# Kernel tuning notes

Hardware: AMD Instinct MI355X
Metric: run time of the kernel (lower is better)

## Reference

```python
import jax, jax.numpy as jnp
import numpy as np

NUM_LAYERS = 5
EMB = 300
N_GRAPHS = 4096
BN_EPS = 1e-5
TEMP = 0.04


def _gnn_encode(x, edge_index, edge_attr, atom_emb1, atom_emb2,
                edge_emb1, edge_emb2, mlp_w1, mlp_b1, mlp_w2, mlp_b2,
                bn_gamma, bn_beta):
    n = x.shape[0]
    h = atom_emb1[x[:, 0]] + atom_emb2[x[:, 1]]  # [N, EMB]
    src, dst = edge_index[0], edge_index[1]
    for l in range(NUM_LAYERS):
        eemb = edge_emb1[l][edge_attr[:, 0]] + edge_emb2[l][edge_attr[:, 1]]  # [E, EMB]
        self_emb = edge_emb1[l][4] + edge_emb2[l][0]  # self-loop edge_attr = [4, 0]
        agg = jax.ops.segment_sum(h[src] + eemb, dst, num_segments=n)
        agg = agg + h + self_emb  # self-loop messages
        h = jax.nn.relu(agg @ mlp_w1[l] + mlp_b1[l]) @ mlp_w2[l] + mlp_b2[l]
        mean = jnp.mean(h, axis=0)
        var = jnp.var(h, axis=0)
        h = (h - mean) / jnp.sqrt(var + BN_EPS) * bn_gamma[l] + bn_beta[l]
        if l != NUM_LAYERS - 1:
            h = jax.nn.relu(h)
    return h


def _branch(x, edge_index, edge_attr, node_batch, params):
    h = _gnn_encode(x, edge_index, edge_attr, *params[:-2])
    h = h @ params[-2] + params[-1]  # projector
    s = jax.ops.segment_sum(h, node_batch, num_segments=N_GRAPHS)
    cnt = jax.ops.segment_sum(jnp.ones((h.shape[0],), h.dtype), node_batch,
                              num_segments=N_GRAPHS)
    g = s / jnp.maximum(cnt, 1.0)[:, None]  # global mean pool
    norm = jnp.maximum(jnp.linalg.norm(g, axis=1, keepdims=True), 1e-12)
    return g / norm


def setup_inputs() -> dict:
    key = jax.random.key(0)
    ks = jax.random.split(key, 24)
    f = jnp.float32
    inp = {}
    inp['x0'] = jax.random.randint(ks[0], (100000, 2), 0, 3)
    inp['edge_index0'] = jax.random.randint(ks[1], (2, 400000), 0, 100000)
    inp['edge_attr0'] = jax.random.randint(ks[2], (400000, 2), 0, 3)
    inp['batch0'] = jnp.sort(jax.random.randint(ks[3], (100000,), 0, N_GRAPHS))
    inp['x1'] = jax.random.randint(ks[4], (100000, 2), 0, 3)
    inp['edge_index1'] = jax.random.randint(ks[5], (2, 400000), 0, 100000)
    inp['edge_attr1'] = jax.random.randint(ks[6], (400000, 2), 0, 3)
    inp['batch1'] = jnp.sort(jax.random.randint(ks[7], (100000,), 0, N_GRAPHS))
    s = 0.02
    inp['atom_emb1'] = jax.random.normal(ks[8], (120, EMB), f) * s
    inp['atom_emb2'] = jax.random.normal(ks[9], (3, EMB), f) * s
    inp['edge_emb1'] = jax.random.normal(ks[10], (NUM_LAYERS, 6, EMB), f) * s
    inp['edge_emb2'] = jax.random.normal(ks[11], (NUM_LAYERS, 3, EMB), f) * s
    inp['mlp_w1'] = jax.random.normal(ks[12], (NUM_LAYERS, EMB, 2 * EMB), f) * s
    inp['mlp_b1'] = jnp.zeros((NUM_LAYERS, 2 * EMB), f)
    inp['mlp_w2'] = jax.random.normal(ks[13], (NUM_LAYERS, 2 * EMB, EMB), f) * s
    inp['mlp_b2'] = jnp.zeros((NUM_LAYERS, EMB), f)
    inp['bn_gamma'] = jnp.ones((NUM_LAYERS, EMB), f)
    inp['bn_beta'] = jnp.zeros((NUM_LAYERS, EMB), f)
    inp['proj_w'] = jax.random.normal(ks[14], (EMB, EMB), f) * s
    inp['proj_b'] = jnp.zeros((EMB,), f)
    return inp


def reference(x0, edge_index0, edge_attr0, batch0,
              x1, edge_index1, edge_attr1, batch1,
              atom_emb1, atom_emb2, edge_emb1, edge_emb2,
              mlp_w1, mlp_b1, mlp_w2, mlp_b2, bn_gamma, bn_beta,
              proj_w, proj_b):
    params = (atom_emb1, atom_emb2, edge_emb1, edge_emb2,
              mlp_w1, mlp_b1, mlp_w2, mlp_b2, bn_gamma, bn_beta,
              proj_w, proj_b)
    f0 = _branch(x0, edge_index0, edge_attr0, batch0, params)
    f1 = _branch(x1, edge_index1, edge_attr1, batch1, params)
    logits = (f0 @ f1.T) / TEMP  # [G, G]
    return logits
```

## Files before the change

### kernel.cpp

```cpp
#include <hip/hip_runtime.h>
#include <hip/hip_bf16.h>


#define EMB 300
#define EMBC 75
#define AGGP 320
#define AGGC 80
#define HID 600
#define NGRAPH 4096
#define BN_EPS 1e-5f
#define INV_TEMP 25.0f
#define NRED 24

typedef __hip_bfloat16 bf16;
struct __align__(8) bf4 { bf16 x, y, z, w; };
typedef __attribute__((ext_vector_type(8))) short short8;
typedef __attribute__((ext_vector_type(4))) float float4v;

__device__ inline float b2f(bf16 v) { return __bfloat162float(v); }
__device__ inline bf16 f2b(float v) { return __float2bfloat16(v); }
__device__ inline unsigned short f2bu(float f) {
    bf16 b = __float2bfloat16(f); unsigned short u; __builtin_memcpy(&u, &b, 2); return u;
}

typedef const unsigned int __attribute__((address_space(1)))* gas_t;
typedef unsigned int __attribute__((address_space(3)))* las_t;
__device__ __forceinline__ void gl_lds16(const unsigned short* g, unsigned short* l) {
    __builtin_amdgcn_global_load_lds((gas_t)g, (las_t)l, 16, 0, 0);
}


__global__ void k_zero_f(float* __restrict__ p, int n) {
    int i = blockIdx.x * blockDim.x + threadIdx.x;
    if (i < n) p[i] = 0.f;
}
__global__ void k_zero_i(int* __restrict__ p, int n) {
    int i = blockIdx.x * blockDim.x + threadIdx.x;
    if (i < n) p[i] = 0;
}


__global__ void k_split(const float* __restrict__ W, int K, int N, int Kpad, int Npad,
                        unsigned short* __restrict__ hi, unsigned short* __restrict__ lo) {
    int idx = blockIdx.x * blockDim.x + threadIdx.x;
    if (idx >= Npad * Kpad) return;
    int n = idx / Kpad, k = idx % Kpad;
    float v = (n < N && k < K) ? W[(size_t)k * N + n] : 0.f;
    bf16 h = __float2bfloat16(v);
    float rem = v - __bfloat162float(h);
    bf16 l = __float2bfloat16(rem);
    unsigned short hu, lu;
    __builtin_memcpy(&hu, &h, 2); __builtin_memcpy(&lu, &l, 2);
    hi[idx] = hu; lo[idx] = lu;
}

__global__ void k_fsplit(const float* __restrict__ f, unsigned short* __restrict__ hi,
                         unsigned short* __restrict__ lo, int G) {
    int idx = blockIdx.x * blockDim.x + threadIdx.x;
    if (idx >= G * AGGP) return;
    int g = idx / AGGP, c = idx % AGGP;
    float v = (c < EMB) ? f[(size_t)g * EMB + c] : 0.f;
    bf16 h = __float2bfloat16(v);
    float rem = v - __bfloat162float(h);
    unsigned short hu; __builtin_memcpy(&hu, &h, 2);
    hi[idx] = hu;
    lo[idx] = f2bu(rem);
}


__global__ void k_hist(const int* __restrict__ ei, int* __restrict__ deg, int E) {
    int e = blockIdx.x * blockDim.x + threadIdx.x;
    if (e < E) atomicAdd(&deg[ei[E + e]], 1);
}

__global__ void k_chunksum(const int* __restrict__ deg, int* __restrict__ csum, int total) {
    __shared__ int s[256];
    int t = threadIdx.x, i = blockIdx.x * 256 + t;
    s[t] = (i < total) ? deg[i] : 0;
    __syncthreads();
    for (int off = 128; off > 0; off >>= 1) {
        if (t < off) s[t] += s[t + off];
        __syncthreads();
    }
    if (t == 0) csum[blockIdx.x] = s[0];
}

__global__ void k_scanchunks(const int* __restrict__ csum, int* __restrict__ coff, int n) {
    if (threadIdx.x == 0) {
        int acc = 0;
        for (int b = 0; b < n; ++b) { coff[b] = acc; acc += csum[b]; }
    }
}

__global__ void k_scan2(const int* __restrict__ deg, const int* __restrict__ coff,
                        int* __restrict__ rowstart, int total) {
    __shared__ int s[256];
    int t = threadIdx.x, b = blockIdx.x, i = b * 256 + t;
    int v = (i < total) ? deg[i] : 0;
    s[t] = v;
    __syncthreads();
    for (int off = 1; off < 256; off <<= 1) {
        int u = (t >= off) ? s[t - off] : 0;
        __syncthreads();
        s[t] += u;
        __syncthreads();
    }
    if (i < total) rowstart[i] = coff[b] + s[t] - v;
}

__global__ void k_initcursor(const int* __restrict__ rowstart, int* __restrict__ cur, int N) {
    int i = blockIdx.x * blockDim.x + threadIdx.x;
    if (i < N) cur[i] = rowstart[i];
}

__global__ void k_fill(const int* __restrict__ ei, int* __restrict__ cur,
                       int* __restrict__ esorted, int E) {
    int e = blockIdx.x * blockDim.x + threadIdx.x;
    if (e < E) {
        int p = atomicAdd(&cur[ei[E + e]], 1);
        esorted[p] = e;
    }
}

__global__ void k_pack(const int* __restrict__ ei, const int* __restrict__ ea,
                       const int* __restrict__ esorted, int* __restrict__ packed, int E) {
    int p = blockIdx.x * blockDim.x + threadIdx.x;
    if (p >= E) return;
    int e = esorted[p];
    int s = ei[e];
    int cb = ea[2 * e] * 3 + ea[2 * e + 1];
    packed[p] = s | (cb << 17);
}

__global__ void k_sortb(const int* __restrict__ rowstart, int* __restrict__ packed, int N) {
    int n = blockIdx.x * blockDim.x + threadIdx.x;
    if (n >= N) return;
    int p0 = rowstart[n], p1 = rowstart[n + 1];
    for (int i = p0 + 1; i < p1; ++i) {
        int v = packed[i];
        int j = i - 1;
        while (j >= p0 && packed[j] > v) { packed[j + 1] = packed[j]; --j; }
        packed[j + 1] = v;
    }
}

__global__ void k_gstart(const int* __restrict__ batch, int* __restrict__ gstart, int N) {
    int g = blockIdx.x * blockDim.x + threadIdx.x;
    if (g > NGRAPH) return;
    int lo = 0, hi = N;
    while (lo < hi) { int mid = (lo + hi) >> 1; if (batch[mid] < g) lo = mid + 1; else hi = mid; }
    gstart[g] = lo;
}

__global__ void k_combo(const float4* __restrict__ e1, const float4* __restrict__ e2,
                        float4* __restrict__ cmb) {
    int t = blockIdx.x * blockDim.x + threadIdx.x;
    if (t >= 18 * EMBC) return;
    int cb = t / EMBC, j = t % EMBC;
    float4 u = e1[(cb / 3) * EMBC + j];
    float4 v = e2[(cb % 3) * EMBC + j];
    float4 r; r.x = u.x + v.x; r.y = u.y + v.y; r.z = u.z + v.z; r.w = u.w + v.w;
    cmb[t] = r;
}


__global__ void k_init_h(const int* __restrict__ x,
                         const float4* __restrict__ ae1,
                         const float4* __restrict__ ae2,
                         bf4* __restrict__ h4, int N) {
    int idx = blockIdx.x * blockDim.x + threadIdx.x;
    if (idx >= N * EMBC) return;
    int i = idx / EMBC, j = idx % EMBC;
    int a0 = x[2 * i], a1 = x[2 * i + 1];
    float4 u = ae1[a0 * EMBC + j];
    float4 v = ae2[a1 * EMBC + j];
    bf4 r = { f2b(u.x + v.x), f2b(u.y + v.y), f2b(u.z + v.z), f2b(u.w + v.w) };
    h4[idx] = r;
}

__global__ void k_aggregate(const bf4* __restrict__ h4,
                            const int* __restrict__ packed,
                            const float4* __restrict__ cmb,
                            const int* __restrict__ rowstart,
                            const float* __restrict__ stats, int use_aff,
                            bf4* __restrict__ agg4, int N) {
    int idx = blockIdx.x * blockDim.x + threadIdx.x;
    if (idx >= N * AGGC) return;
    int n = idx / AGGC, j = idx % AGGC;
    if (j >= EMBC) {
        bf4 z = { f2b(0.f), f2b(0.f), f2b(0.f), f2b(0.f) };
        agg4[idx] = z;
        return;
    }
    float4 sc = make_float4(1.f, 1.f, 1.f, 1.f);
    float4 sh = make_float4(0.f, 0.f, 0.f, 0.f);
    if (use_aff) {
        sc = ((const float4*)stats)[j];
        sh = ((const float4*)(stats + EMB))[j];
    }
    bf4 hv = h4[(size_t)n * EMBC + j];
    float hx = b2f(hv.x), hy = b2f(hv.y), hz = b2f(hv.z), hw = b2f(hv.w);
    if (use_aff) {
        hx = fmaxf(hx * sc.x + sh.x, 0.f); hy = fmaxf(hy * sc.y + sh.y, 0.f);
        hz = fmaxf(hz * sc.z + sh.z, 0.f); hw = fmaxf(hw * sc.w + sh.w, 0.f);
    }
    float4 s0 = cmb[12 * EMBC + j];
    float ax = hx + s0.x, ay = hy + s0.y, az = hz + s0.z, aw = hw + s0.w;
    int p0 = rowstart[n], p1 = rowstart[n + 1];
    for (int p = p0; p < p1; ++p) {
        int u = packed[p];
        int s = u & 131071;
        int cb = u >> 17;
        bf4 hs = h4[(size_t)s * EMBC + j];
        float gx = b2f(hs.x), gy = b2f(hs.y), gz = b2f(hs.z), gw = b2f(hs.w);
        if (use_aff) {
            gx = fmaxf(gx * sc.x + sh.x, 0.f); gy = fmaxf(gy * sc.y + sh.y, 0.f);
            gz = fmaxf(gz * sc.z + sh.z, 0.f); gw = fmaxf(gw * sc.w + sh.w, 0.f);
        }
        float4 cv = cmb[cb * EMBC + j];
        ax += gx + cv.x; ay += gy + cv.y;
        az += gz + cv.z; aw += gw + cv.w;
    }
    bf4 r = { f2b(ax), f2b(ay), f2b(az), f2b(aw) };
    agg4[idx] = r;
}

__global__ void k_bncopy(const bf4* __restrict__ h4, const float* __restrict__ stats,
                         bf4* __restrict__ dst, int N) {
    int idx = blockIdx.x * blockDim.x + threadIdx.x;
    if (idx >= N * AGGC) return;
    int n = idx / AGGC, j = idx % AGGC;
    if (j >= EMBC) {
        bf4 z = { f2b(0.f), f2b(0.f), f2b(0.f), f2b(0.f) };
        dst[idx] = z;
        return;
    }
    float4 sc = ((const float4*)stats)[j];
    float4 sh = ((const float4*)(stats + EMB))[j];
    bf4 v = h4[(size_t)n * EMBC + j];
    bf4 r = { f2b(b2f(v.x) * sc.x + sh.x), f2b(b2f(v.y) * sc.y + sh.y),
              f2b(b2f(v.z) * sc.z + sh.z), f2b(b2f(v.w) * sc.w + sh.w) };
    dst[idx] = r;
}


#define GBM 128
#define GBN 64
#define GBK 32

__global__ __launch_bounds__(256, 5)
void k_gemm_mfma(const unsigned short* __restrict__ A, int lda, int Kpad,
                 const unsigned short* __restrict__ Bhi,
                 const unsigned short* __restrict__ Blo, int ldb,
                 const float* __restrict__ bias,
                 unsigned short* __restrict__ C, int ldc, int M, int Nc, int relu,
                 float* __restrict__ psum, int do_stats) {
    __shared__ unsigned short As[2][GBM][GBK];
    __shared__ unsigned short Bh[2][GBN][GBK];
    __shared__ unsigned short Bl[2][GBN][GBK];

    int tid = threadIdx.x;
    int wv = tid >> 6, lane = tid & 63;
    int quad = lane >> 4, l16 = lane & 15;
    int wm = wv & 1, wn = wv >> 1;

    int srow = lane >> 2;
    int gch = (lane & 3) ^ ((lane >> 3) & 3);
    int pc = quad ^ ((l16 >> 1) & 3);

    int ncols = gridDim.x, nrows = gridDim.y;
    int lin = blockIdx.y * ncols + blockIdx.x;
    int g = lin / (8 * ncols);
    int rem = lin - g * 8 * ncols;
    int rows_in = min(8, nrows - g * 8);
    int colb = rem / rows_in;
    int rowb = g * 8 + (rem - colb * rows_in);
    int row0 = rowb * GBM;
    int col0 = colb * GBN;

    const unsigned short* Asrc[2];
    #pragma unroll
    for (int j = 0; j < 2; ++j) {
        int r = 32 * wv + 16 * j + srow;
        Asrc[j] = A + (size_t)min(row0 + r, M - 1) * lda + gch * 8;
    }
    const unsigned short* Bsrc = Bhi + (size_t)(col0 + 16 * wv + srow) * ldb + gch * 8;
    const size_t dBL = (size_t)(Blo - Bhi);

    float4v acc[4][2];
    #pragma unroll
    for (int i = 0; i < 4; ++i)
        #pragma unroll
        for (int j = 0; j < 2; ++j) acc[i][j] = (float4v){0.f, 0.f, 0.f, 0.f};

    const int ntk = Kpad / GBK;

    gl_lds16(Asrc[0], &As[0][32 * wv][0]);
    gl_lds16(Asrc[1], &As[0][32 * wv + 16][0]);
    gl_lds16(Bsrc, &Bh[0][16 * wv][0]);
    gl_lds16(Bsrc + dBL, &Bl[0][16 * wv][0]);
    if (ntk > 1) {
        gl_lds16(Asrc[0] + GBK, &As[1][32 * wv][0]);
        gl_lds16(Asrc[1] + GBK, &As[1][32 * wv + 16][0]);
        gl_lds16(Bsrc + GBK, &Bh[1][16 * wv][0]);
        gl_lds16(Bsrc + GBK + dBL, &Bl[1][16 * wv][0]);
    }

    for (int t = 0; t < ntk; ++t) {
        int cur = t & 1;
        if (t + 1 < ntk) {
            asm volatile("s_waitcnt vmcnt(4)" ::: "memory");
        } else {
            asm volatile("s_waitcnt vmcnt(0)" ::: "memory");
        }
        __builtin_amdgcn_s_barrier();
        __builtin_amdgcn_sched_barrier(0);
        short8 a[4];
        #pragma unroll
        for (int mt = 0; mt < 4; ++mt)
            a[mt] = *(const short8*)(&As[cur][64 * wm + mt * 16 + l16][pc * 8]);
        #pragma unroll
        for (int ntl = 0; ntl < 2; ++ntl) {
            short8 bh = *(const short8*)(&Bh[cur][32 * wn + ntl * 16 + l16][pc * 8]);
            short8 bl = *(const short8*)(&Bl[cur][32 * wn + ntl * 16 + l16][pc * 8]);
            #pragma unroll
            for (int mt = 0; mt < 4; ++mt) {
                acc[mt][ntl] = __builtin_amdgcn_mfma_f32_16x16x32_bf16(a[mt], bh, acc[mt][ntl], 0, 0, 0);
                acc[mt][ntl] = __builtin_amdgcn_mfma_f32_16x16x32_bf16(a[mt], bl, acc[mt][ntl], 0, 0, 0);
            }
        }
        __builtin_amdgcn_s_barrier();
        __builtin_amdgcn_sched_barrier(0);
        if (t + 2 < ntk) {
            int k2 = (t + 2) * GBK;
            gl_lds16(Asrc[0] + k2, &As[cur][32 * wv][0]);
            gl_lds16(Asrc[1] + k2, &As[cur][32 * wv + 16][0]);
            gl_lds16(Bsrc + k2, &Bh[cur][16 * wv][0]);
            gl_lds16(Bsrc + k2 + dBL, &Bl[cur][16 * wv][0]);
        }
    }

    float sv[2], qv[2];
    #pragma unroll
    for (int ntl = 0; ntl < 2; ++ntl) { sv[ntl] = 0.f; qv[ntl] = 0.f; }
    #pragma unroll
    for (int mt = 0; mt < 4; ++mt) {
        int rbase = row0 + 64 * wm + mt * 16 + quad * 4;
        #pragma unroll
        for (int ntl = 0; ntl < 2; ++ntl) {
            int c = col0 + 32 * wn + ntl * 16 + l16;
            if (c >= Nc) continue;
            float bs = bias[c];
            #pragma unroll
            for (int i = 0; i < 4; ++i) {
                int r = rbase + i;
                if (r >= M) continue;
                float v = acc[mt][ntl][i] + bs;
                if (relu) v = fmaxf(v, 0.f);
                if (do_stats) { sv[ntl] += v; qv[ntl] += v * v; }
                C[(size_t)r * ldc + c] = f2bu(v);
            }
        }
    }
    if (do_stats) {
        float* cred = (float*)(&As[0][0][0]);
        #pragma unroll
        for (int ntl = 0; ntl < 2; ++ntl) {
            float s = sv[ntl], q = qv[ntl];
            s += __shfl_down(s, 32, 64); s += __shfl_down(s, 16, 64);
            q += __shfl_down(q, 32, 64); q += __shfl_down(q, 16, 64);
            if (quad == 0) {
                cred[wv * 64 + ntl * 16 + l16] = s;
                cred[256 + wv * 64 + ntl * 16 + l16] = q;
            }
        }
        __syncthreads();
        if (tid < 64) {
            int gc = tid >> 5, cin = tid & 31;
            float s = cred[(2 * gc) * 64 + cin] + cred[(2 * gc + 1) * 64 + cin];
            float q = cred[256 + (2 * gc) * 64 + cin] + cred[256 + (2 * gc + 1) * 64 + cin];
            int c = col0 + tid;
            psum[(size_t)rowb * 768 + c] = s;
            psum[(size_t)rowb * 768 + 384 + c] = q;
        }
    }
}


__global__ __launch_bounds__(256)
void k_logits(const unsigned short* __restrict__ Ahg, const unsigned short* __restrict__ Alg,
              const unsigned short* __restrict__ Bhg, const unsigned short* __restrict__ Blg,
              float* __restrict__ C, float scale) {
    __shared__ unsigned short sAh[64][64];
    __shared__ unsigned short sAl[64][64];
    __shared__ unsigned short sBh[128][64];
    __shared__ unsigned short sBl[128][64];

    int tid = threadIdx.x;
    int wv = tid >> 6, lane = tid & 63;
    int quad = lane >> 4, l16 = lane & 15;
    int lrow = lane >> 3;
    int gchunk = (lane & 7) ^ lrow;
    int sw = lane & 7;
    int row0 = blockIdx.y * 64;
    int col0 = blockIdx.x * 128;

    float4v acc[8];
    #pragma unroll
    for (int j = 0; j < 8; ++j) acc[j] = (float4v){0.f, 0.f, 0.f, 0.f};

    for (int k0 = 0; k0 < AGGP; k0 += 64) {
        #pragma unroll
        for (int j = 0; j < 2; ++j) {
            int r = 16 * wv + 8 * j + lrow;
            size_t go = (size_t)(row0 + r) * AGGP + k0 + gchunk * 8;
            gl_lds16(Ahg + go, &sAh[16 * wv + 8 * j][0]);
            gl_lds16(Alg + go, &sAl[16 * wv + 8 * j][0]);
        }
        #pragma unroll
        for (int j = 0; j < 4; ++j) {
            int r = 32 * wv + 8 * j + lrow;
            size_t go = (size_t)(col0 + r) * AGGP + k0 + gchunk * 8;
            gl_lds16(Bhg + go, &sBh[32 * wv + 8 * j][0]);
            gl_lds16(Blg + go, &sBl[32 * wv + 8 * j][0]);
        }
        __syncthreads();

        #pragma unroll
        for (int ks = 0; ks < 64; ks += 32) {
            int pcl = ((ks >> 3) + quad) ^ sw;
            short8 ah = *(const short8*)(&sAh[wv * 16 + l16][pcl * 8]);
            short8 al = *(const short8*)(&sAl[wv * 16 + l16][pcl * 8]);
            #pragma unroll
            for (int nt = 0; nt < 8; ++nt) {
                short8 bh = *(const short8*)(&sBh[nt * 16 + l16][pcl * 8]);
                short8 bl = *(const short8*)(&sBl[nt * 16 + l16][pcl * 8]);
                acc[nt] = __builtin_amdgcn_mfma_f32_16x16x32_bf16(ah, bh, acc[nt], 0, 0, 0);
                acc[nt] = __builtin_amdgcn_mfma_f32_16x16x32_bf16(ah, bl, acc[nt], 0, 0, 0);
                acc[nt] = __builtin_amdgcn_mfma_f32_16x16x32_bf16(al, bh, acc[nt], 0, 0, 0);
            }
        }
        __syncthreads();
    }

    int rbase = row0 + wv * 16 + quad * 4;
    #pragma unroll
    for (int nt = 0; nt < 8; ++nt) {
        int c = col0 + nt * 16 + l16;
        #pragma unroll
        for (int i = 0; i < 4; ++i)
            C[(size_t)(rbase + i) * NGRAPH + c] = acc[nt][i] * scale;
    }
}


__global__ void k_statred(const float* __restrict__ psum, float* __restrict__ part2, int nrb) {
    int b = blockIdx.x, c = threadIdx.x;
    float acc = 0.f;
    for (int r = b; r < nrb; r += NRED) acc += psum[(size_t)r * 768 + c];
    part2[b * 768 + c] = acc;
}

__global__ void k_bn_prep(const float* __restrict__ part2, float* __restrict__ stats,
                          const float* __restrict__ gamma, const float* __restrict__ beta,
                          float invN) {
    int c = threadIdx.x;
    if (c >= EMB) return;
    float s = 0.f, q = 0.f;
    for (int b = 0; b < NRED; ++b) {
        s += part2[b * 768 + c];
        q += part2[b * 768 + 384 + c];
    }
    float mean = s * invN;
    float var = q * invN - mean * mean;
    float scale = gamma[c] * rsqrtf(var + BN_EPS);
    stats[c] = scale;
    stats[EMB + c] = beta[c] - mean * scale;
}


__global__ void k_poolnorm(const bf16* __restrict__ proj, const int* __restrict__ gstart,
                           float* __restrict__ f) {
    int g = blockIdx.x, t = threadIdx.x;
    int s = gstart[g], e = gstart[g + 1];
    float sum = 0.f;
    if (t < EMB)
        for (int r = s; r < e; ++r) sum += b2f(proj[(size_t)r * AGGP + t]);
    float cnt = fmaxf((float)(e - s), 1.f);
    float m = sum / cnt;
    float q = (t < EMB) ? m * m : 0.f;
    for (int off = 32; off > 0; off >>= 1) q += __shfl_down(q, off, 64);
    __shared__ float red[5];
    int lane = t & 63, wid = t >> 6;
    if (lane == 0) red[wid] = q;
    __syncthreads();
    float tot = red[0] + red[1] + red[2] + red[3] + red[4];
    float invn = 1.f / fmaxf(sqrtf(tot), 1e-12f);
    if (t < EMB) f[(size_t)g * EMB + t] = m * invn;
}


static inline int ceil_div(int a, int b) { return (a + b - 1) / b; }

extern "C" void kernel_launch(void* const* d_in, const int* in_sizes, int n_in,
                              void* d_out, int out_size, void* d_ws, size_t ws_size,
                              hipStream_t stream) {
    const int N = in_sizes[0] / 2;
    const int E = in_sizes[1] / 2;

    const int* x[2]  = { (const int*)d_in[0], (const int*)d_in[4] };
    const int* ei[2] = { (const int*)d_in[1], (const int*)d_in[5] };
    const int* ea[2] = { (const int*)d_in[2], (const int*)d_in[6] };
    const int* bt[2] = { (const int*)d_in[3], (const int*)d_in[7] };
    const float* atom1 = (const float*)d_in[8];
    const float* atom2 = (const float*)d_in[9];
    const float* ee1 = (const float*)d_in[10];
    const float* ee2 = (const float*)d_in[11];
    const float* w1  = (const float*)d_in[12];
    const float* b1  = (const float*)d_in[13];
    const float* w2  = (const float*)d_in[14];
    const float* b2  = (const float*)d_in[15];
    const float* gam = (const float*)d_in[16];
    const float* bet = (const float*)d_in[17];
    const float* pw  = (const float*)d_in[18];
    const float* pb  = (const float*)d_in[19];
    float* out = (float*)d_out;

    char* wsb = (char*)d_ws;
    bf16* h    = (bf16*)(wsb);
    bf16* agg  = (bf16*)(wsb + 60000000);
    bf16* hid  = (bf16*)(wsb + 124000000);
    float* guard = (float*)(wsb + 244000000);
    float* f0  = (float*)(wsb + 244000256);
    float* f1  = (float*)(wsb + 248915456);
    unsigned short* f0hi = (unsigned short*)(wsb + 124000000);
    unsigned short* f0lo = (unsigned short*)(wsb + 126621440);
    unsigned short* f1hi = (unsigned short*)(wsb + 129242880);
    unsigned short* f1lo = (unsigned short*)(wsb + 131864320);

    int* deg      = (int*)d_out;
    int* rowstart = deg + (N + 1);
    int* cursor   = rowstart + (N + 1);
    int* esorted  = cursor + N;
    int* packed   = esorted + E;
    int* csum     = packed + E;
    int* coff     = csum + 512;
    int* gstart   = coff + 512;
    float* stats  = (float*)(gstart + 4097);
    float* cmb    = stats + 600;
    char* splits  = (char*)d_out + 4500224;
    unsigned short* w1hi = (unsigned short*)(splits);
    unsigned short* w1lo = (unsigned short*)(splits + 2048000);
    unsigned short* w2hi = (unsigned short*)(splits + 4096000);
    unsigned short* w2lo = (unsigned short*)(splits + 6553600);
    unsigned short* pjhi = (unsigned short*)(splits + 9011200);
    unsigned short* pjlo = (unsigned short*)(splits + 9256960);
    float* psum  = (float*)((char*)d_out + 20971520);
    float* part2 = (float*)((char*)d_out + 25165824);

    const int TB = 256;
    const int nh_blocks = ceil_div(N * EMBC, TB);
    const int na_blocks = ceil_div(N * AGGC, TB);
    const int nchunks = ceil_div(N + 1, 256);
    const float invN = 1.f / (float)N;

    k_zero_f<<<1, 64, 0, stream>>>(guard, 64);

    for (int l = 0; l < 5; ++l) {
        k_split<<<ceil_div(640 * 320, TB), TB, 0, stream>>>(
            w1 + (size_t)l * EMB * HID, EMB, HID, 320, 640,
            w1hi + (size_t)l * 640 * 320, w1lo + (size_t)l * 640 * 320);
        k_split<<<ceil_div(384 * 640, TB), TB, 0, stream>>>(
            w2 + (size_t)l * HID * EMB, HID, EMB, 640, 384,
            w2hi + (size_t)l * 384 * 640, w2lo + (size_t)l * 384 * 640);
    }
    k_split<<<ceil_div(384 * 320, TB), TB, 0, stream>>>(pw, EMB, EMB, 320, 384, pjhi, pjlo);

    const int mrows = ceil_div(N, GBM);
    dim3 g1(10, mrows);
    dim3 g2(6, mrows);
    dim3 glg(32, 64);

    for (int br = 0; br < 2; ++br) {
        float* fout = br == 0 ? f0 : f1;
        k_zero_i<<<ceil_div(N + 1, TB), TB, 0, stream>>>(deg, N + 1);
        k_hist<<<ceil_div(E, TB), TB, 0, stream>>>(ei[br], deg, E);
        k_chunksum<<<nchunks, 256, 0, stream>>>(deg, csum, N + 1);
        k_scanchunks<<<1, 64, 0, stream>>>(csum, coff, nchunks);
        k_scan2<<<nchunks, 256, 0, stream>>>(deg, coff, rowstart, N + 1);
        k_initcursor<<<ceil_div(N, TB), TB, 0, stream>>>(rowstart, cursor, N);
        k_fill<<<ceil_div(E, TB), TB, 0, stream>>>(ei[br], cursor, esorted, E);
        k_pack<<<ceil_div(E, TB), TB, 0, stream>>>(ei[br], ea[br], esorted, packed, E);
        k_sortb<<<ceil_div(N, TB), TB, 0, stream>>>(rowstart, packed, N);
        k_gstart<<<ceil_div(NGRAPH + 1, TB), TB, 0, stream>>>(bt[br], gstart, N);
        k_init_h<<<nh_blocks, TB, 0, stream>>>(x[br], (const float4*)atom1,
                                               (const float4*)atom2, (bf4*)h, N);
        for (int l = 0; l < 5; ++l) {
            k_combo<<<ceil_div(18 * EMBC, TB), TB, 0, stream>>>(
                (const float4*)(ee1 + (size_t)l * 6 * EMB),
                (const float4*)(ee2 + (size_t)l * 3 * EMB), (float4*)cmb);
            k_aggregate<<<na_blocks, TB, 0, stream>>>((const bf4*)h, packed,
                                                      (const float4*)cmb, rowstart,
                                                      stats, l > 0, (bf4*)agg, N);
            k_gemm_mfma<<<g1, 256, 0, stream>>>(
                (const unsigned short*)agg, AGGP, AGGP,
                w1hi + (size_t)l * 640 * 320, w1lo + (size_t)l * 640 * 320, 320,
                b1 + (size_t)l * HID, (unsigned short*)hid, HID, N, HID, 1,
                nullptr, 0);
            k_gemm_mfma<<<g2, 256, 0, stream>>>(
                (const unsigned short*)hid, HID, 640,
                w2hi + (size_t)l * 384 * 640, w2lo + (size_t)l * 384 * 640, 640,
                b2 + (size_t)l * EMB, (unsigned short*)h, EMB, N, EMB, 0,
                psum, 1);
            k_statred<<<NRED, 768, 0, stream>>>(psum, part2, mrows);
            k_bn_prep<<<1, 320, 0, stream>>>(part2, stats, gam + (size_t)l * EMB,
                                             bet + (size_t)l * EMB, invN);
        }
        k_bncopy<<<na_blocks, TB, 0, stream>>>((const bf4*)h, stats, (bf4*)hid, N);
        k_gemm_mfma<<<g2, 256, 0, stream>>>(
            (const unsigned short*)hid, AGGP, AGGP,
            pjhi, pjlo, 320, pb, (unsigned short*)agg, AGGP, N, EMB, 0,
            nullptr, 0);
        k_poolnorm<<<NGRAPH, 320, 0, stream>>>(agg, gstart, fout);
    }
    k_fsplit<<<ceil_div(NGRAPH * AGGP, TB), TB, 0, stream>>>(f0, f0hi, f0lo, NGRAPH);
    k_fsplit<<<ceil_div(NGRAPH * AGGP, TB), TB, 0, stream>>>(f1, f1hi, f1lo, NGRAPH);
    k_logits<<<glg, 256, 0, stream>>>(f0hi, f0lo, f1hi, f1lo, out, INV_TEMP);
}
```

Baseline: 4.610 ms.

## Load GEMM B fragments directly into registers instead of staging through LDS

The B operand tiles (hi and lo bf16 split) are no longer staged in shared memory. Each wave now loads its own MFMA B fragments straight from global memory into registers, prefetched one k-step ahead. The A pipeline drops from a two-stage-ahead prefetch with manual vmcnt waits to a one-ahead prefetch synchronized with __syncthreads, and launch bounds drop from 5 to 4 blocks per CU to make room for the extra registers. This cuts LDS traffic and footprint, but B data is now read redundantly by both wm waves through global or L2, prefetch depth is shallower, and occupancy is lower.

```diff
diff --git a/kernel.cpp b/kernel.cpp
--- a/kernel.cpp
+++ b/kernel.cpp
@@ -248,7 +248,7 @@
 #define GBN 64
 #define GBK 32
 
-__global__ __launch_bounds__(256, 5)
+__global__ __launch_bounds__(256, 4)
 void k_gemm_mfma(const unsigned short* __restrict__ A, int lda, int Kpad,
                  const unsigned short* __restrict__ Bhi,
                  const unsigned short* __restrict__ Blo, int ldb,
@@ -256,8 +256,6 @@
                  unsigned short* __restrict__ C, int ldc, int M, int Nc, int relu,
                  float* __restrict__ psum, int do_stats) {
     __shared__ unsigned short As[2][GBM][GBK];
-    __shared__ unsigned short Bh[2][GBN][GBK];
-    __shared__ unsigned short Bl[2][GBN][GBK];
 
     int tid = threadIdx.x;
     int wv = tid >> 6, lane = tid & 63;
@@ -278,13 +276,16 @@
     int row0 = rowb * GBM;
     int col0 = colb * GBN;
 
-    const unsigned short* Asrc[2];
-    #pragma unroll
-    for (int j = 0; j < 2; ++j) {
-        int r = 32 * wv + 16 * j + srow;
-        Asrc[j] = A + (size_t)min(row0 + r, M - 1) * lda + gch * 8;
-    }
-    const unsigned short* Bsrc = Bhi + (size_t)(col0 + 16 * wv + srow) * ldb + gch * 8;
+    const unsigned short* Asrc0;
+    const unsigned short* Asrc1;
+    {
+        int r0 = 32 * wv + srow;
+        int r1 = 32 * wv + 16 + srow;
+        Asrc0 = A + (size_t)min(row0 + r0, M - 1) * lda + gch * 8;
+        Asrc1 = A + (size_t)min(row0 + r1, M - 1) * lda + gch * 8;
+    }
+    const unsigned short* Bp0 = Bhi + (size_t)(col0 + 32 * wn + l16) * ldb + quad * 8;
+    const unsigned short* Bp1 = Bhi + (size_t)(col0 + 32 * wn + 16 + l16) * ldb + quad * 8;
     const size_t dBL = (size_t)(Blo - Bhi);
 
     float4v acc[4][2];
@@ -295,49 +296,42 @@
 
     const int ntk = Kpad / GBK;
 
-    gl_lds16(Asrc[0], &As[0][32 * wv][0]);
-    gl_lds16(Asrc[1], &As[0][32 * wv + 16][0]);
-    gl_lds16(Bsrc, &Bh[0][16 * wv][0]);
-    gl_lds16(Bsrc + dBL, &Bl[0][16 * wv][0]);
-    if (ntk > 1) {
-        gl_lds16(Asrc[0] + GBK, &As[1][32 * wv][0]);
-        gl_lds16(Asrc[1] + GBK, &As[1][32 * wv + 16][0]);
-        gl_lds16(Bsrc + GBK, &Bh[1][16 * wv][0]);
-        gl_lds16(Bsrc + GBK + dBL, &Bl[1][16 * wv][0]);
-    }
+    gl_lds16(Asrc0, &As[0][32 * wv][0]);
+    gl_lds16(Asrc1, &As[0][32 * wv + 16][0]);
+    short8 bc0 = *(const short8*)(Bp0);
+    short8 bc1 = *(const short8*)(Bp0 + dBL);
+    short8 bc2 = *(const short8*)(Bp1);
+    short8 bc3 = *(const short8*)(Bp1 + dBL);
+    __syncthreads();
 
     for (int t = 0; t < ntk; ++t) {
         int cur = t & 1;
+        short8 bn0, bn1, bn2, bn3;
         if (t + 1 < ntk) {
-            asm volatile("s_waitcnt vmcnt(4)" ::: "memory");
-        } else {
-            asm volatile("s_waitcnt vmcnt(0)" ::: "memory");
-        }
-        __builtin_amdgcn_s_barrier();
-        __builtin_amdgcn_sched_barrier(0);
+            int k1 = (t + 1) * GBK;
+            gl_lds16(Asrc0 + k1, &As[cur ^ 1][32 * wv][0]);
+            gl_lds16(Asrc1 + k1, &As[cur ^ 1][32 * wv + 16][0]);
+            bn0 = *(const short8*)(Bp0 + k1);
+            bn1 = *(const short8*)(Bp0 + k1 + dBL);
+            bn2 = *(const short8*)(Bp1 + k1);
+            bn3 = *(const short8*)(Bp1 + k1 + dBL);
+        }
         short8 a[4];
         #pragma unroll
         for (int mt = 0; mt < 4; ++mt)
             a[mt] = *(const short8*)(&As[cur][64 * wm + mt * 16 + l16][pc * 8]);
         #pragma unroll
-        for (int ntl = 0; ntl < 2; ++ntl) {
-            short8 bh = *(const short8*)(&Bh[cur][32 * wn + ntl * 16 + l16][pc * 8]);
-            short8 bl = *(const short8*)(&Bl[cur][32 * wn + ntl * 16 + l16][pc * 8]);
-            #pragma unroll
-            for (int mt = 0; mt < 4; ++mt) {
-                acc[mt][ntl] = __builtin_amdgcn_mfma_f32_16x16x32_bf16(a[mt], bh, acc[mt][ntl], 0, 0, 0);
-                acc[mt][ntl] = __builtin_amdgcn_mfma_f32_16x16x32_bf16(a[mt], bl, acc[mt][ntl], 0, 0, 0);
-            }
-        }
-        __builtin_amdgcn_s_barrier();
-        __builtin_amdgcn_sched_barrier(0);
-        if (t + 2 < ntk) {
-            int k2 = (t + 2) * GBK;
-            gl_lds16(Asrc[0] + k2, &As[cur][32 * wv][0]);
-            gl_lds16(Asrc[1] + k2, &As[cur][32 * wv + 16][0]);
-            gl_lds16(Bsrc + k2, &Bh[cur][16 * wv][0]);
-            gl_lds16(Bsrc + k2 + dBL, &Bl[cur][16 * wv][0]);
-        }
+        for (int mt = 0; mt < 4; ++mt) {
+            acc[mt][0] = __builtin_amdgcn_mfma_f32_16x16x32_bf16(a[mt], bc0, acc[mt][0], 0, 0, 0);
+            acc[mt][0] = __builtin_amdgcn_mfma_f32_16x16x32_bf16(a[mt], bc1, acc[mt][0], 0, 0, 0);
+        }
+        #pragma unroll
+        for (int mt = 0; mt < 4; ++mt) {
+            acc[mt][1] = __builtin_amdgcn_mfma_f32_16x16x32_bf16(a[mt], bc2, acc[mt][1], 0, 0, 0);
+            acc[mt][1] = __builtin_amdgcn_mfma_f32_16x16x32_bf16(a[mt], bc3, acc[mt][1], 0, 0, 0);
+        }
+        __syncthreads();
+        bc0 = bn0; bc1 = bn1; bc2 = bn2; bc3 = bn3;
     }
 
     float sv[2], qv[2];
```

Result: slower. 6.354 ms (+37.8%).
